# Performance work log

Hardware: AMD Instinct MI355X
Metric: run time of the kernel (lower is better)

The kernel has to match this reference:

```python
import jax, jax.numpy as jnp
import numpy as np
from jax import lax

B, S, E, H = 4, 1024, 512, 8
D = E // H


def setup_inputs() -> dict:
    key = jax.random.key(0)
    k1, k2, k3 = jax.random.split(key, 3)
    source = jax.random.normal(k1, (B, S, E), dtype=jnp.float32)
    target = jax.random.normal(k2, (B, S, E), dtype=jnp.float32)
    # orthogonal-initialized positional encoder [1, H, 1, D]; random rows are a fine stand-in
    enc = jax.random.normal(k3, (1, H, 1, D), dtype=jnp.float32)
    enc = enc / jnp.linalg.norm(enc, axis=-1, keepdims=True)
    return {
        "source": source,
        "target": target,
        "encoder": enc,
        "alpha": jnp.float32(1.0),
        "beta": jnp.float32(1.0),
        "gamma": jnp.float32(2.0),
    }


def _split_heads(x):
    b, s, e = x.shape
    return x.reshape(b, s, H, e // H).transpose(0, 2, 1, 3)  # [B,H,S,D]


def reference(source, target, encoder, alpha, beta, gamma):
    q = _split_heads(source)  # [B,H,S,D]
    k = _split_heads(target)  # [B,H,S,D]
    pe = encoder[0, :, 0, :]  # [H,D]

    # --- grammar (time) attention: sequential tanh recurrence over t ---
    def step(cc, k_t):
        # cc, k_t: [B,H,D]
        cc = jnp.tanh(cc * pe)
        out = jnp.einsum('bhsd,bhd->bhs', q, cc)  # [B,H,S]
        return k_t * cc, out  # decay_rate = 0.0

    cc0 = k[:, :, 0, :]                      # initial cumulative context
    k_ts = jnp.moveaxis(k, 2, 0)             # [S,B,H,D]
    _, outs = lax.scan(step, cc0, k_ts)      # outs: [S,B,H,S]
    grammar = jnp.moveaxis(outs, 0, 3) / jnp.sqrt(jnp.float32(D))  # [B,H,S,S]
    grammar = jax.nn.softmax(grammar, axis=-1)

    # --- semantic attention ---
    semantic = jnp.einsum('bhsd,bhtd->bhst', q, k) / 100.0  # [B,H,S,S]

    w = jax.nn.softmax((alpha * semantic + beta * grammar) / gamma, axis=-1)

    # merge_heads: [B,H,S,S] -> [B,S,H*S]
    wm = w.transpose(0, 2, 1, 3).reshape(B, S, H * S)
    # output: wm^T @ target -> [B, H*S, E]
    return jnp.matmul(wm.transpose(0, 2, 1), target)
```

## Files before the change

kernel.cpp:

```cpp
#include <hip/hip_runtime.h>
#include <hip/hip_bf16.h>
#include <stdint.h>

#define S_LEN 1024
#define E_DIM 512
#define H_NUM 8
#define D_DIM 64
#define B_NUM 4
#define BH_NUM 32

using s16x8 = __attribute__((ext_vector_type(8))) short;
using f32x4 = __attribute__((ext_vector_type(4))) float;
using us4   = __attribute__((ext_vector_type(4))) unsigned short;

static __device__ __forceinline__ unsigned short f2bf(float f) {
  __hip_bfloat16 h = __float2bfloat16(f);
  return __builtin_bit_cast(unsigned short, h);
}
static __device__ __forceinline__ float bf2f(unsigned short u) {
  return __bfloat162float(__builtin_bit_cast(__hip_bfloat16, u));
}

#define NB_RECUR 8
#define NB_PACK  2048
#define NB_TR    512

__global__ __launch_bounds__(256) void k_prep(const float* __restrict__ src,
                                              const float* __restrict__ tgt,
                                              const float* __restrict__ enc,
                                              __hip_bfloat16* __restrict__ qb,
                                              __hip_bfloat16* __restrict__ kb,
                                              __hip_bfloat16* __restrict__ cb,
                                              __hip_bfloat16* __restrict__ tT) {
  __shared__ float tile[64][65];
  const int bid = blockIdx.x;
  const int tid = threadIdx.x;

  if (bid < NB_RECUR) {
    int g = bid * 256 + tid;
    int d = g & 63;
    int bh = g >> 6;
    int h = bh & 7;
    int b = bh >> 3;
    float pe = enc[h * D_DIM + d];
    float pe2 = 2.0f * pe;
    const float* tp = tgt + (size_t)b * S_LEN * E_DIM + h * D_DIM + d;
    __hip_bfloat16* cp = cb + (size_t)bh * S_LEN * D_DIM + d;

    constexpr int CH = 32;
    float bufA[CH], bufB[CH];
#pragma unroll
    for (int i = 0; i < CH; ++i) bufA[i] = tp[(size_t)i * E_DIM];
    float cc = bufA[0];

#pragma unroll 1
    for (int ch = 0; ch < S_LEN / CH; ch += 2) {
      if (ch + 1 < S_LEN / CH) {
#pragma unroll
        for (int i = 0; i < CH; ++i)
          bufB[i] = tp[(size_t)((ch + 1) * CH + i) * E_DIM];
      }
#pragma unroll
      for (int i = 0; i < CH; ++i) {
        float m = cc * pe2;
        float e = __expf(-fabsf(m));
        float th = __builtin_copysignf((1.0f - e) * __builtin_amdgcn_rcpf(1.0f + e), m);
        cp[(size_t)(ch * CH + i) * D_DIM] = __float2bfloat16(th);
        cc = bufA[i] * th;
      }
      if (ch + 2 < S_LEN / CH) {
#pragma unroll
        for (int i = 0; i < CH; ++i)
          bufA[i] = tp[(size_t)((ch + 2) * CH + i) * E_DIM];
      }
#pragma unroll
      for (int i = 0; i < CH; ++i) {
        float m = cc * pe2;
        float e = __expf(-fabsf(m));
        float th = __builtin_copysignf((1.0f - e) * __builtin_amdgcn_rcpf(1.0f + e), m);
        cp[(size_t)((ch + 1) * CH + i) * D_DIM] = __float2bfloat16(th);
        cc = bufB[i] * th;
      }
    }
  } else if (bid < NB_RECUR + NB_PACK) {
    size_t i4 = ((size_t)(bid - NB_RECUR) * 256 + tid) * 4;
    float4 s4 = *reinterpret_cast<const float4*>(src + i4);
    float4 t4 = *reinterpret_cast<const float4*>(tgt + i4);
    int e = (int)(i4 & 511);
    size_t bs = i4 >> 9;
    int s = (int)(bs & 1023);
    int b = (int)(bs >> 10);
    int h = e >> 6, d = e & 63;
    size_t o = (((size_t)(b * H_NUM + h) * S_LEN) + s) * D_DIM + d;
    us4 qv = {f2bf(s4.x), f2bf(s4.y), f2bf(s4.z), f2bf(s4.w)};
    us4 kv = {f2bf(t4.x), f2bf(t4.y), f2bf(t4.z), f2bf(t4.w)};
    *reinterpret_cast<us4*>(qb + o) = qv;
    *reinterpret_cast<us4*>(kb + o) = kv;
  } else {
    int lb = bid - (NB_RECUR + NB_PACK);
    int sx = lb & 15, ey = (lb >> 4) & 7, b = lb >> 7;
    int e0 = ey * 64, s0 = sx * 64;
    int tx = tid & 63, ty = tid >> 6;
    const float* p = tgt + ((size_t)b * S_LEN + s0) * E_DIM + e0;
#pragma unroll
    for (int r = ty; r < 64; r += 4) tile[r][tx] = p[(size_t)r * E_DIM + tx];
    __syncthreads();
    __hip_bfloat16* q = tT + ((size_t)b * E_DIM + e0) * S_LEN + s0;
#pragma unroll
    for (int r = ty; r < 64; r += 4) q[(size_t)r * S_LEN + tx] = __float2bfloat16(tile[tx][r]);
  }
}

__global__ __launch_bounds__(256) void k_weights(const __hip_bfloat16* __restrict__ qb,
                                                 const __hip_bfloat16* __restrict__ kb,
                                                 const __hip_bfloat16* __restrict__ cb,
                                                 __hip_bfloat16* __restrict__ wt,
                                                 const float* __restrict__ pal,
                                                 const float* __restrict__ pbe,
                                                 const float* __restrict__ pga) {
  __shared__ float red0[4][16];
  __shared__ float red1[4][16];

  const int tid = threadIdx.x;
  const int wave = tid >> 6, lane = tid & 63;
  const int quad = lane >> 4, col = lane & 15;

  const int g = blockIdx.x;
  const int xcd = g & 7;
  const int r = g >> 3;
  const int bh = xcd * 4 + (r >> 6);
  const int s0 = (r & 63) * 16;

  const float alpha = pal[0], beta = pbe[0];
  const float inv_gamma = 1.0f / pga[0];
  const float sa = alpha * 0.01f * inv_gamma;
  const float sb = beta * inv_gamma;

  const __hip_bfloat16* qrow = qb + ((size_t)bh * S_LEN + s0 + col) * D_DIM;
  s16x8 a0 = *reinterpret_cast<const s16x8*>(qrow + quad * 8);
  s16x8 a1 = *reinterpret_cast<const s16x8*>(qrow + 32 + quad * 8);

  const int t_base = wave * 256;
  uint32_t stg[16][2];
  float    stk[16][4];

  const __hip_bfloat16* cbh = cb + ((size_t)bh * S_LEN + t_base + col) * D_DIM;
  const __hip_bfloat16* kbh = kb + ((size_t)bh * S_LEN + t_base + col) * D_DIM;
  float lg[4] = {0.f, 0.f, 0.f, 0.f};
#pragma unroll
  for (int it = 0; it < 16; ++it) {
    const __hip_bfloat16* crow = cbh + (size_t)it * 16 * D_DIM;
    const __hip_bfloat16* krow = kbh + (size_t)it * 16 * D_DIM;
    s16x8 cb0 = *reinterpret_cast<const s16x8*>(crow + quad * 8);
    s16x8 cb1 = *reinterpret_cast<const s16x8*>(crow + 32 + quad * 8);
    s16x8 kb0 = *reinterpret_cast<const s16x8*>(krow + quad * 8);
    s16x8 kb1 = *reinterpret_cast<const s16x8*>(krow + 32 + quad * 8);
    f32x4 dg = {0.f, 0.f, 0.f, 0.f};
    dg = __builtin_amdgcn_mfma_f32_16x16x32_bf16(a0, cb0, dg, 0, 0, 0);
    dg = __builtin_amdgcn_mfma_f32_16x16x32_bf16(a1, cb1, dg, 0, 0, 0);
    f32x4 dk = {0.f, 0.f, 0.f, 0.f};
    dk = __builtin_amdgcn_mfma_f32_16x16x32_bf16(a0, kb0, dk, 0, 0, 0);
    dk = __builtin_amdgcn_mfma_f32_16x16x32_bf16(a1, kb1, dk, 0, 0, 0);
    uint32_t p0 = 0, p1 = 0;
#pragma unroll
    for (int i = 0; i < 4; ++i) {
      float gv = __expf(dg[i] * 0.125f);
      unsigned short u = f2bf(gv);
      lg[i] += bf2f(u);
      if (i < 2) p0 |= (uint32_t)u << (16 * i);
      else       p1 |= (uint32_t)u << (16 * (i - 2));
      stk[it][i] = dk[i];
    }
    stg[it][0] = p0;
    stg[it][1] = p1;
  }
#pragma unroll
  for (int m = 1; m < 16; m <<= 1) {
#pragma unroll
    for (int i = 0; i < 4; ++i) lg[i] += __shfl_xor(lg[i], m);
  }
  if (col == 0) {
#pragma unroll
    for (int i = 0; i < 4; ++i) red0[wave][quad * 4 + i] = lg[i];
  }
  __syncthreads();
  float ilg[4];
#pragma unroll
  for (int i = 0; i < 4; ++i) {
    int rr = quad * 4 + i;
    ilg[i] = 1.0f / (red0[0][rr] + red0[1][rr] + red0[2][rr] + red0[3][rr]);
  }

  float lw[4] = {0.f, 0.f, 0.f, 0.f};
#pragma unroll
  for (int it = 0; it < 16; ++it) {
#pragma unroll
    for (int i = 0; i < 4; ++i) {
      unsigned short u = (unsigned short)((i < 2 ? stg[it][0] >> (16 * i)
                                                 : stg[it][1] >> (16 * (i - 2))) & 0xffffu);
      float gv = bf2f(u) * ilg[i];
      float z = sa * stk[it][i] + sb * gv;
      float wv = __expf(z);
      stk[it][i] = wv;
      lw[i] += wv;
    }
  }
#pragma unroll
  for (int m = 1; m < 16; m <<= 1) {
#pragma unroll
    for (int i = 0; i < 4; ++i) lw[i] += __shfl_xor(lw[i], m);
  }
  if (col == 0) {
#pragma unroll
    for (int i = 0; i < 4; ++i) red1[wave][quad * 4 + i] = lw[i];
  }
  __syncthreads();
  float ilw[4];
#pragma unroll
  for (int i = 0; i < 4; ++i) {
    int rr = quad * 4 + i;
    ilw[i] = 1.0f / (red1[0][rr] + red1[1][rr] + red1[2][rr] + red1[3][rr]);
  }

  __hip_bfloat16* wrow = wt + ((size_t)bh * S_LEN + t_base + col) * S_LEN + s0 + quad * 4;
#pragma unroll
  for (int it = 0; it < 16; ++it) {
    us4 o;
#pragma unroll
    for (int i = 0; i < 4; ++i) o[i] = f2bf(stk[it][i] * ilw[i]);
    *reinterpret_cast<us4*>(wrow + (size_t)it * 16 * S_LEN) = o;
  }
}

typedef const __attribute__((address_space(1))) uint32_t gas_uint;
typedef __attribute__((address_space(3))) uint32_t las_uint;

__global__ __launch_bounds__(256) void k_outgemm(const __hip_bfloat16* __restrict__ wt,
                                                 const __hip_bfloat16* __restrict__ tT,
                                                 float* __restrict__ out) {
  __shared__ __hip_bfloat16 As[128 * 64];
  __shared__ __hip_bfloat16 Bs[128 * 64];
  const int tid = threadIdx.x;
  const int wave = tid >> 6, lane = tid & 63;
  const int quad = lane >> 4, col = lane & 15;

  const int g = blockIdx.x;
  const int xcd = g & 7;
  const int local = g >> 3;
  const int strip = xcd * 32 + (local >> 2);
  const int ntile = local & 3;
  const int bh = strip >> 3;
  const int mt = strip & 7;
  const int b = bh >> 3;
  const int m0 = mt * 128;
  const int n0 = ntile * 128;

  const __hip_bfloat16* Ag = wt + (size_t)bh * S_LEN * S_LEN;
  const __hip_bfloat16* Bg = tT + (size_t)b * E_DIM * S_LEN;
  const int mw = (wave >> 1) * 64, nw = (wave & 1) * 64;
  const int lrow = lane >> 3;
  const int lcol = (lane & 7) * 8;

  f32x4 acc[4][4];
#pragma unroll
  for (int i = 0; i < 4; ++i)
#pragma unroll
    for (int j = 0; j < 4; ++j) acc[i][j] = (f32x4){0.f, 0.f, 0.f, 0.f};

  for (int kt = 0; kt < 16; ++kt) {
    const int k0 = kt * 64;
    __syncthreads();
#pragma unroll
    for (int j = 0; j < 4; ++j) {
      int row = j * 32 + wave * 8 + lrow;
      const __hip_bfloat16* gp = Ag + (size_t)(m0 + row) * S_LEN + k0 + lcol;
      __builtin_amdgcn_global_load_lds((gas_uint*)gp,
                                       (las_uint*)(As + (j * 32 + wave * 8) * 64),
                                       16, 0, 0);
    }
#pragma unroll
    for (int j = 0; j < 4; ++j) {
      int row = j * 32 + wave * 8 + lrow;
      const __hip_bfloat16* gp = Bg + (size_t)(n0 + row) * S_LEN + k0 + lcol;
      __builtin_amdgcn_global_load_lds((gas_uint*)gp,
                                       (las_uint*)(Bs + (j * 32 + wave * 8) * 64),
                                       16, 0, 0);
    }
    __syncthreads();
#pragma unroll
    for (int ks = 0; ks < 2; ++ks) {
      s16x8 af[4], bf[4];
#pragma unroll
      for (int i = 0; i < 4; ++i)
        af[i] = *reinterpret_cast<const s16x8*>(As + (mw + i * 16 + col) * 64 + ks * 32 + quad * 8);
#pragma unroll
      for (int i = 0; i < 4; ++i)
        bf[i] = *reinterpret_cast<const s16x8*>(Bs + (nw + i * 16 + col) * 64 + ks * 32 + quad * 8);
#pragma unroll
      for (int mi = 0; mi < 4; ++mi)
#pragma unroll
        for (int ni = 0; ni < 4; ++ni)
          acc[mi][ni] = __builtin_amdgcn_mfma_f32_16x16x32_bf16(af[mi], bf[ni], acc[mi][ni], 0, 0, 0);
    }
  }

#pragma unroll
  for (int mi = 0; mi < 4; ++mi)
#pragma unroll
    for (int ni = 0; ni < 4; ++ni)
#pragma unroll
      for (int i = 0; i < 4; ++i) {
        int m = m0 + mw + mi * 16 + quad * 4 + i;
        int n = n0 + nw + ni * 16 + col;
        out[((size_t)bh * S_LEN + m) * E_DIM + n] = acc[mi][ni][i];
      }
}

extern "C" void kernel_launch(void* const* d_in, const int* in_sizes, int n_in,
                              void* d_out, int out_size, void* d_ws, size_t ws_size,
                              hipStream_t stream) {
  (void)in_sizes; (void)n_in; (void)out_size; (void)ws_size;
  const float* src = (const float*)d_in[0];
  const float* tgt = (const float*)d_in[1];
  const float* enc = (const float*)d_in[2];
  const float* pal = (const float*)d_in[3];
  const float* pbe = (const float*)d_in[4];
  const float* pga = (const float*)d_in[5];
  float* out = (float*)d_out;

  char* ws = (char*)d_ws;
  __hip_bfloat16* qb = (__hip_bfloat16*)(ws);
  __hip_bfloat16* kb = (__hip_bfloat16*)(ws + ((size_t)4 << 20));
  __hip_bfloat16* cb = (__hip_bfloat16*)(ws + ((size_t)8 << 20));
  __hip_bfloat16* tT = (__hip_bfloat16*)(ws + ((size_t)12 << 20));
  __hip_bfloat16* wt = (__hip_bfloat16*)(ws + ((size_t)16 << 20));

  k_prep<<<NB_RECUR + NB_PACK + NB_TR, 256, 0, stream>>>(src, tgt, enc, qb, kb, cb, tT);
  k_weights<<<dim3((S_LEN / 16) * BH_NUM), 256, 0, stream>>>(qb, kb, cb, wt, pal, pbe, pga);
  k_outgemm<<<dim3((E_DIM / 128) * (S_LEN / 128) * BH_NUM), 256, 0, stream>>>(wt, tT, out);
}
```

Baseline: 247.5 us.

## Stage k_weights key/context tiles through LDS with async triple-buffered loads

Replaces direct per-lane global vector loads of the context and key rows in k_weights with global_load_lds async copies into a per-wave triple-buffered LDS stage, prefetching two iterations ahead and using an XOR swizzle to avoid bank conflicts. MFMAs then read fragments from LDS, and s_setprio raises priority around the MFMA group. The aim is to hide global load latency behind compute. The cost is 48KB of added LDS per block, which may reduce occupancy, and manual vmcnt waits that must match the number of loads in flight.

```diff
diff --git a/kernel.cpp b/kernel.cpp
--- a/kernel.cpp
+++ b/kernel.cpp
@@ -12,6 +12,9 @@
 using s16x8 = __attribute__((ext_vector_type(8))) short;
 using f32x4 = __attribute__((ext_vector_type(4))) float;
 using us4   = __attribute__((ext_vector_type(4))) unsigned short;
+
+typedef const __attribute__((address_space(1))) uint32_t gas_uint;
+typedef __attribute__((address_space(3))) uint32_t las_uint;
 
 static __device__ __forceinline__ unsigned short f2bf(float f) {
   __hip_bfloat16 h = __float2bfloat16(f);
@@ -118,6 +121,7 @@
                                                  const float* __restrict__ pal,
                                                  const float* __restrict__ pbe,
                                                  const float* __restrict__ pga) {
+  __shared__ unsigned short stage[4][3][2048];
   __shared__ float red0[4][16];
   __shared__ float red1[4][16];
 
@@ -144,23 +148,45 @@
   uint32_t stg[16][2];
   float    stk[16][4];
 
-  const __hip_bfloat16* cbh = cb + ((size_t)bh * S_LEN + t_base + col) * D_DIM;
-  const __hip_bfloat16* kbh = kb + ((size_t)bh * S_LEN + t_base + col) * D_DIM;
+  const char* cbase = (const char*)(cb + ((size_t)bh * S_LEN + t_base) * D_DIM);
+  const char* kbase = (const char*)(kb + ((size_t)bh * S_LEN + t_base) * D_DIM);
+  const int so0 = ((lane >> 3) << 7) | (((lane & 7) ^ ((lane >> 3) & 7)) << 4);
+
+  auto stage_it = [&](int it) {
+    unsigned short* db = &stage[wave][it % 3][0];
+    const char* cs = cbase + it * 2048;
+    const char* ks = kbase + it * 2048;
+    __builtin_amdgcn_global_load_lds((gas_uint*)(cs + so0),        (las_uint*)(db),        16, 0, 0);
+    __builtin_amdgcn_global_load_lds((gas_uint*)(cs + so0 + 1024), (las_uint*)(db + 512),  16, 0, 0);
+    __builtin_amdgcn_global_load_lds((gas_uint*)(ks + so0),        (las_uint*)(db + 1024), 16, 0, 0);
+    __builtin_amdgcn_global_load_lds((gas_uint*)(ks + so0 + 1024), (las_uint*)(db + 1536), 16, 0, 0);
+  };
+
+  stage_it(0);
+  stage_it(1);
+
+  const int xswz = (col & 7) << 4;
   float lg[4] = {0.f, 0.f, 0.f, 0.f};
 #pragma unroll
   for (int it = 0; it < 16; ++it) {
-    const __hip_bfloat16* crow = cbh + (size_t)it * 16 * D_DIM;
-    const __hip_bfloat16* krow = kbh + (size_t)it * 16 * D_DIM;
-    s16x8 cb0 = *reinterpret_cast<const s16x8*>(crow + quad * 8);
-    s16x8 cb1 = *reinterpret_cast<const s16x8*>(crow + 32 + quad * 8);
-    s16x8 kb0 = *reinterpret_cast<const s16x8*>(krow + quad * 8);
-    s16x8 kb1 = *reinterpret_cast<const s16x8*>(krow + 32 + quad * 8);
+    if (it < 15) asm volatile("s_waitcnt vmcnt(4)" ::: "memory");
+    else         asm volatile("s_waitcnt vmcnt(0)" ::: "memory");
+    const char* cw = (const char*)&stage[wave][it % 3][0];
+    const char* kw = cw + 2048;
+    const int rb = col * 128;
+    s16x8 cf0 = *reinterpret_cast<const s16x8*>(cw + rb + ((quad * 16) ^ xswz));
+    s16x8 cf1 = *reinterpret_cast<const s16x8*>(cw + rb + ((64 + quad * 16) ^ xswz));
+    s16x8 kf0 = *reinterpret_cast<const s16x8*>(kw + rb + ((quad * 16) ^ xswz));
+    s16x8 kf1 = *reinterpret_cast<const s16x8*>(kw + rb + ((64 + quad * 16) ^ xswz));
     f32x4 dg = {0.f, 0.f, 0.f, 0.f};
-    dg = __builtin_amdgcn_mfma_f32_16x16x32_bf16(a0, cb0, dg, 0, 0, 0);
-    dg = __builtin_amdgcn_mfma_f32_16x16x32_bf16(a1, cb1, dg, 0, 0, 0);
     f32x4 dk = {0.f, 0.f, 0.f, 0.f};
-    dk = __builtin_amdgcn_mfma_f32_16x16x32_bf16(a0, kb0, dk, 0, 0, 0);
-    dk = __builtin_amdgcn_mfma_f32_16x16x32_bf16(a1, kb1, dk, 0, 0, 0);
+    __builtin_amdgcn_s_setprio(1);
+    dg = __builtin_amdgcn_mfma_f32_16x16x32_bf16(a0, cf0, dg, 0, 0, 0);
+    dg = __builtin_amdgcn_mfma_f32_16x16x32_bf16(a1, cf1, dg, 0, 0, 0);
+    dk = __builtin_amdgcn_mfma_f32_16x16x32_bf16(a0, kf0, dk, 0, 0, 0);
+    dk = __builtin_amdgcn_mfma_f32_16x16x32_bf16(a1, kf1, dk, 0, 0, 0);
+    __builtin_amdgcn_s_setprio(0);
+    if (it + 2 < 16) stage_it(it + 2);
     uint32_t p0 = 0, p1 = 0;
 #pragma unroll
     for (int i = 0; i < 4; ++i) {
@@ -231,9 +257,6 @@
     *reinterpret_cast<us4*>(wrow + (size_t)it * 16 * S_LEN) = o;
   }
 }
-
-typedef const __attribute__((address_space(1))) uint32_t gas_uint;
-typedef __attribute__((address_space(3))) uint32_t las_uint;
 
 __global__ __launch_bounds__(256) void k_outgemm(const __hip_bfloat16* __restrict__ wt,
                                                  const __hip_bfloat16* __restrict__ tT,
```

Measured after the change: 215.4 us. 13.0% less time.
